# Kernel optimization log

Measured on AMD Instinct MI355X. Metric: run time of the kernel, lower is better.

Reference implementation:

```python
import jax, jax.numpy as jnp
import numpy as np


def setup_inputs() -> dict:
    key = jax.random.key(0)
    k1, k2, k3 = jax.random.split(key, 3)
    N, D, H, E = 8192, 1024, 1024, 16
    scale = 1.0 / np.sqrt(D)
    return {
        "x": jax.random.normal(k1, (N, D), dtype=jnp.float32),
        "router_w": jax.random.normal(k2, (D, E), dtype=jnp.float32) * scale,
        "router_b": jnp.zeros((E,), dtype=jnp.float32),
        "expert_w": jax.random.normal(k3, (E, D, H), dtype=jnp.float32) * scale,
        "expert_b": jnp.zeros((E, H), dtype=jnp.float32),
        "k": 2,
    }


def reference(x, router_w, router_b, expert_w, expert_b, k):
    # Router: softmax over experts, then top-k.
    logits = x @ router_w + router_b                      # [N, E]
    routing_weights = jax.nn.softmax(logits, axis=-1)     # [N, E]
    top_k_weights, top_k_indices = jax.lax.top_k(routing_weights, k)  # [N, k]

    # Dense all-expert compute (faithful to original): [N, E, H]
    expert_outputs = jnp.einsum('nd,edh->neh', x, expert_w) + expert_b[None, :, :]

    # Gather top-k expert outputs: [N, k, H]
    gathered = jnp.take_along_axis(expert_outputs, top_k_indices[:, :, None], axis=1)

    # Weighted sum over k (weights NOT renormalized, as in the original).
    out = jnp.sum(top_k_weights[:, :, None] * gathered, axis=1)  # [N, H]
    return out
```

## Files before the change

kernel.cpp:

```cpp
#include <hip/hip_runtime.h>
#include <hip/hip_bf16.h>


#define N_TOK 8192
#define D_DIM 1024
#define H_DIM 1024
#define E_NUM 16
#define CAP   1024
#define KPAD  40

typedef __attribute__((ext_vector_type(4))) float f32x4;
typedef __attribute__((ext_vector_type(8))) short bf16x8;

__device__ __forceinline__ unsigned short f2bf(float f) {
    unsigned int u = __float_as_uint(f);
    unsigned int r = u + 0x7fffu + ((u >> 16) & 1u);
    return (unsigned short)(r >> 16);
}
__device__ __forceinline__ unsigned int pk2bf(float lo, float hi) {
    return (unsigned int)f2bf(lo) | ((unsigned int)f2bf(hi) << 16);
}

__global__ __launch_bounds__(256, 4) void router_kernel(
    const float* __restrict__ x,
    const float* __restrict__ rw,
    const float* __restrict__ rb,
    int4* __restrict__ res)
{
    const int wave = threadIdx.x >> 6;
    const int lane = threadIdx.x & 63;
    const int ds   = lane >> 4;
    const int e    = lane & 15;
    const int t0   = blockIdx.x * 8 + wave * 2;

    const float* x0  = x + (size_t)t0 * D_DIM + ds * 256;
    const float* x1  = x0 + D_DIM;
    const float* rwp = rw + ds * 4096 + e;

    double acc0 = 0.0, acc1 = 0.0;
#pragma unroll 2
    for (int g = 0; g < 8; ++g) {
        float s0 = 0.0f, s1 = 0.0f;
#pragma unroll
        for (int u = 0; u < 8; ++u) {
            const int jb = g * 8 + u;
            const float4 a = *(const float4*)(x0 + jb * 4);
            const float4 b = *(const float4*)(x1 + jb * 4);
            const float w0 = rwp[jb * 64];
            const float w1 = rwp[jb * 64 + 16];
            const float w2 = rwp[jb * 64 + 32];
            const float w3 = rwp[jb * 64 + 48];
            s0 = fmaf(a.w, w3, fmaf(a.z, w2, fmaf(a.y, w1, fmaf(a.x, w0, s0))));
            s1 = fmaf(b.w, w3, fmaf(b.z, w2, fmaf(b.y, w1, fmaf(b.x, w0, s1))));
        }
        acc0 += (double)s0;
        acc1 += (double)s1;
    }

    double v0 = acc0, v1 = acc1;
    v0 += __shfl_xor(v0, 16); v0 += __shfl_xor(v0, 32);
    v1 += __shfl_xor(v1, 16); v1 += __shfl_xor(v1, 32);

    __shared__ double lg[4][2][E_NUM];
    if (ds == 0) {
        const double bias = (double)rb[e];
        lg[wave][0][e] = v0 + bias;
        lg[wave][1][e] = v1 + bias;
    }
    __syncthreads();

    if (lane < 2) {
        const double* L = lg[wave][lane];
        double m = L[0];
#pragma unroll
        for (int k = 1; k < E_NUM; ++k) m = fmax(m, L[k]);

        int e1 = 0;
#pragma unroll
        for (int k = 1; k < E_NUM; ++k) if (L[k] > L[e1]) e1 = k;
        int e2 = (e1 == 0) ? 1 : 0;
        for (int k = 0; k < E_NUM; ++k)
            if (k != e1 && L[k] > L[e2]) e2 = k;

        float s = 0.0f;
#pragma unroll
        for (int k = 0; k < E_NUM; ++k) s = fmaf(expf((float)(L[k] - m)), 1.0f, s);
        const float w1 = expf((float)(L[e1] - m)) / s;
        const float w2 = expf((float)(L[e2] - m)) / s;

        const int n = t0 + lane;
        res[n] = make_int4(e1, e2, __float_as_int(w1), __float_as_int(w2));
    }
}

__global__ __launch_bounds__(256) void build_lists(
    const int4* __restrict__ res,
    int* __restrict__ counts0, int* __restrict__ counts1,
    int2* __restrict__ entries0, int2* __restrict__ entries1)
{
    const int e = blockIdx.x;
    __shared__ int c0, c1;
    if (threadIdx.x == 0) { c0 = 0; c1 = 0; }
    __syncthreads();

    for (int i = threadIdx.x; i < N_TOK; i += 256) {
        const int4 r = res[i];
        if (r.x == e) {
            int p = atomicAdd(&c0, 1);
            if (p < CAP) entries0[e * CAP + p] = make_int2(i, r.z);
        }
        if (r.y == e) {
            int p = atomicAdd(&c1, 1);
            if (p < CAP) entries1[e * CAP + p] = make_int2(i, r.w);
        }
    }
    __syncthreads();
    if (threadIdx.x == 0) { counts0[e] = c0; counts1[e] = c1; }
}

template <bool ADD>
__global__ __launch_bounds__(256) void moe_mfma_kernel(
    const float* __restrict__ x,
    const float* __restrict__ ew,
    const float* __restrict__ eb,
    const int* __restrict__ counts,
    const int2* __restrict__ entries,
    float* __restrict__ out)
{
    const int flat = blockIdx.x;
    const int lid  = (flat & 7) * 128 + (flat >> 3);
    const int h0 = (lid & 7) * 128;
    const int i0 = ((lid >> 3) & 7) * 128;
    const int e  = lid >> 6;

    int count = counts[e];
    if (count > CAP) count = CAP;
    if (i0 >= count) return;

    __shared__ unsigned short Xs[2][128][KPAD];
    __shared__ unsigned short Ws[2][128][KPAD];
    __shared__ int   s_tok[128];
    __shared__ float s_w[128];

    const int tid = threadIdx.x;
    if (tid < 128) {
        const int i = i0 + tid;
        if (i < count) {
            int2 en = entries[e * CAP + i];
            s_tok[tid] = en.x;
            s_w[tid] = __int_as_float(en.y);
        } else {
            s_tok[tid] = 0;
            s_w[tid] = 0.0f;
        }
    }
    __syncthreads();

    const int wave = tid >> 6;
    const int lane = tid & 63;
    const int wr = (wave >> 1) * 64;
    const int wc = (wave & 1) * 64;
    const int l15 = lane & 15;
    const int quad = lane >> 4;

    f32x4 acc[4][4] = {};

    const int a_kq = (tid & 7) * 4;
    const int a_r0 = tid >> 3;
    const int b_n  = tid & 127;
    const int b_dh = (tid >> 7) * 16;

    const float* ap[4];
#pragma unroll
    for (int it = 0; it < 4; ++it)
        ap[it] = x + (size_t)s_tok[a_r0 + it * 32] * D_DIM + a_kq;
    const float* bp = ew + (size_t)e * D_DIM * H_DIM
                    + (size_t)b_dh * H_DIM + h0 + b_n;

    float4 pa[4];
    float  pb[16];
#pragma unroll
    for (int it = 0; it < 4; ++it) pa[it] = *(const float4*)(ap[it]);
#pragma unroll
    for (int i = 0; i < 16; ++i)  pb[i] = bp[(size_t)i * H_DIM];

    {
#pragma unroll
        for (int it = 0; it < 4; ++it) {
            ushort4 p;
            p.x = f2bf(pa[it].x); p.y = f2bf(pa[it].y);
            p.z = f2bf(pa[it].z); p.w = f2bf(pa[it].w);
            *(ushort4*)&Xs[0][a_r0 + it * 32][a_kq] = p;
        }
        uint4 lo, hi;
        lo.x = pk2bf(pb[0], pb[1]);   lo.y = pk2bf(pb[2], pb[3]);
        lo.z = pk2bf(pb[4], pb[5]);   lo.w = pk2bf(pb[6], pb[7]);
        hi.x = pk2bf(pb[8], pb[9]);   hi.y = pk2bf(pb[10], pb[11]);
        hi.z = pk2bf(pb[12], pb[13]); hi.w = pk2bf(pb[14], pb[15]);
        *(uint4*)&Ws[0][b_n][b_dh]     = lo;
        *(uint4*)&Ws[0][b_n][b_dh + 8] = hi;
    }

    int cur = 0;
    for (int d0 = 0; d0 < D_DIM; d0 += 32) {
        __syncthreads();
        const bool more = (d0 + 32 < D_DIM);

        if (more) {
#pragma unroll
            for (int it = 0; it < 4; ++it)
                pa[it] = *(const float4*)(ap[it] + d0 + 32);
#pragma unroll
            for (int i = 0; i < 16; ++i)
                pb[i] = bp[(size_t)(d0 + 32 + i) * H_DIM];
        }

        bf16x8 af[4], bq[4];
#pragma unroll
        for (int i = 0; i < 4; ++i)
            af[i] = *(const bf16x8*)&Xs[cur][wr + i * 16 + l15][quad * 8];
#pragma unroll
        for (int j = 0; j < 4; ++j)
            bq[j] = *(const bf16x8*)&Ws[cur][wc + j * 16 + l15][quad * 8];
#pragma unroll
        for (int i = 0; i < 4; ++i)
#pragma unroll
            for (int j = 0; j < 4; ++j)
                acc[i][j] = __builtin_amdgcn_mfma_f32_16x16x32_bf16(
                    af[i], bq[j], acc[i][j], 0, 0, 0);

        if (more) {
            const int nxt = cur ^ 1;
#pragma unroll
            for (int it = 0; it < 4; ++it) {
                ushort4 p;
                p.x = f2bf(pa[it].x); p.y = f2bf(pa[it].y);
                p.z = f2bf(pa[it].z); p.w = f2bf(pa[it].w);
                *(ushort4*)&Xs[nxt][a_r0 + it * 32][a_kq] = p;
            }
            uint4 lo, hi;
            lo.x = pk2bf(pb[0], pb[1]);   lo.y = pk2bf(pb[2], pb[3]);
            lo.z = pk2bf(pb[4], pb[5]);   lo.w = pk2bf(pb[6], pb[7]);
            hi.x = pk2bf(pb[8], pb[9]);   hi.y = pk2bf(pb[10], pb[11]);
            hi.z = pk2bf(pb[12], pb[13]); hi.w = pk2bf(pb[14], pb[15]);
            *(uint4*)&Ws[nxt][b_n][b_dh]     = lo;
            *(uint4*)&Ws[nxt][b_n][b_dh + 8] = hi;
        }
        cur ^= 1;
    }

    float bias_j[4];
    const float* ebp = eb + e * H_DIM + h0 + wc;
#pragma unroll
    for (int j = 0; j < 4; ++j) bias_j[j] = ebp[j * 16 + l15];

#pragma unroll
    for (int i = 0; i < 4; ++i) {
#pragma unroll
        for (int r = 0; r < 4; ++r) {
            const int row = wr + i * 16 + quad * 4 + r;
            if (i0 + row < count) {
                const int tok = s_tok[row];
                const float w = s_w[row];
                float* op = out + (size_t)tok * H_DIM + h0 + wc + l15;
#pragma unroll
                for (int j = 0; j < 4; ++j) {
                    float v = w * (acc[i][j][r] + bias_j[j]);
                    if (ADD) v += op[j * 16];
                    op[j * 16] = v;
                }
            }
        }
    }
}

extern "C" void kernel_launch(void* const* d_in, const int* in_sizes, int n_in,
                              void* d_out, int out_size, void* d_ws, size_t ws_size,
                              hipStream_t stream)
{
    const float* x  = (const float*)d_in[0];
    const float* rw = (const float*)d_in[1];
    const float* rb = (const float*)d_in[2];
    const float* ew = (const float*)d_in[3];
    const float* eb = (const float*)d_in[4];

    char* ws = (char*)d_ws;
    int*  counts0  = (int*)ws;
    int*  counts1  = (int*)(ws + 64);
    int2* entries0 = (int2*)(ws + 1024);
    int2* entries1 = (int2*)(ws + 1024 + E_NUM * CAP * 8);

    int4* res = (int4*)d_out;

    router_kernel<<<N_TOK / 8, 256, 0, stream>>>(x, rw, rb, res);

    build_lists<<<E_NUM, 256, 0, stream>>>(res, counts0, counts1,
                                           entries0, entries1);

    moe_mfma_kernel<false><<<1024, 256, 0, stream>>>(
        x, ew, eb, counts0, entries0, (float*)d_out);
    moe_mfma_kernel<true><<<1024, 256, 0, stream>>>(
        x, ew, eb, counts1, entries1, (float*)d_out);
}
```

Baseline: 330.4 us.

## Pre-convert inputs and transposed expert weights to bf16 before grouped GEMM

Adds a conversion kernel that writes x as bf16 and each expert's weight matrix transposed to bf16 in workspace. The expert GEMMs then load pre-converted bf16 tiles directly instead of converting fp32 to bf16 inside the inner loop. Blocks are assigned only to occupied expert tiles through a prefix walk over the counts. This adds an extra full pass over x and all expert weights (about 96MB read, 48MB written) and needs a large workspace; otherwise it falls back to the old path.

```diff
diff --git a/kernel.cpp b/kernel.cpp
--- a/kernel.cpp
+++ b/kernel.cpp
@@ -116,6 +116,181 @@
     }
     __syncthreads();
     if (threadIdx.x == 0) { counts0[e] = c0; counts1[e] = c1; }
+}
+
+__global__ __launch_bounds__(256) void cvt_kernel(
+    const float* __restrict__ x,
+    const float* __restrict__ ew,
+    unsigned short* __restrict__ xb,
+    unsigned short* __restrict__ wt)
+{
+    const int tid = threadIdx.x;
+    if (blockIdx.x < 4096) {
+        const size_t base = ((size_t)blockIdx.x * 256 + tid) * 8;
+        const float4 a = *(const float4*)(x + base);
+        const float4 b = *(const float4*)(x + base + 4);
+        uint4 p;
+        p.x = pk2bf(a.x, a.y); p.y = pk2bf(a.z, a.w);
+        p.z = pk2bf(b.x, b.y); p.w = pk2bf(b.z, b.w);
+        *(uint4*)(xb + base) = p;
+        return;
+    }
+    __shared__ unsigned short Ts[64][68];
+    const int wi = blockIdx.x - 4096;
+    const int e  = wi >> 8;
+    const int kt = (wi >> 4) & 15;
+    const int ht = wi & 15;
+
+    {
+        const int kl0 = tid >> 4;
+        const int hl  = (tid & 15) * 4;
+        const float* src = ew + (size_t)e * (D_DIM * H_DIM)
+                         + (size_t)(kt * 64 + kl0) * H_DIM + ht * 64 + hl;
+#pragma unroll
+        for (int i = 0; i < 4; ++i) {
+            const float4 v = *(const float4*)(src + (size_t)i * 16 * H_DIM);
+            ushort4 p;
+            p.x = f2bf(v.x); p.y = f2bf(v.y); p.z = f2bf(v.z); p.w = f2bf(v.w);
+            *(ushort4*)&Ts[kl0 + i * 16][hl] = p;
+        }
+    }
+    __syncthreads();
+    {
+        const int h2 = tid >> 2;
+        const int kc = (tid & 3) * 16;
+        unsigned int r[8];
+#pragma unroll
+        for (int i = 0; i < 8; ++i)
+            r[i] = (unsigned int)Ts[kc + 2 * i][h2]
+                 | ((unsigned int)Ts[kc + 2 * i + 1][h2] << 16);
+        unsigned short* dst = wt + (size_t)e * (D_DIM * H_DIM)
+                            + (size_t)(ht * 64 + h2) * D_DIM + kt * 64 + kc;
+        *(uint4*)dst       = *(uint4*)&r[0];
+        *(uint4*)(dst + 8) = *(uint4*)&r[4];
+    }
+}
+
+template <bool ADD>
+__global__ __launch_bounds__(256) void moe_gemm_bf16(
+    const unsigned short* __restrict__ xb,
+    const unsigned short* __restrict__ wt,
+    const float* __restrict__ eb,
+    const int* __restrict__ counts,
+    const int2* __restrict__ entries,
+    float* __restrict__ out)
+{
+    int e = 0, loc = blockIdx.x, count = 0;
+    for (; e < E_NUM; ++e) {
+        int c = counts[e]; if (c > CAP) c = CAP;
+        const int nb = ((c + 127) >> 7) << 3;
+        if (loc < nb) { count = c; break; }
+        loc -= nb;
+    }
+    if (e == E_NUM) return;
+    const int i0 = (loc >> 3) * 128;
+    const int h0 = (loc & 7) * 128;
+
+    __shared__ unsigned short Xs[2][128][KPAD];
+    __shared__ unsigned short Ws[2][128][KPAD];
+    __shared__ int   s_tok[128];
+    __shared__ float s_w[128];
+
+    const int tid = threadIdx.x;
+    if (tid < 128) {
+        const int i = i0 + tid;
+        if (i < count) {
+            int2 en = entries[e * CAP + i];
+            s_tok[tid] = en.x;
+            s_w[tid] = __int_as_float(en.y);
+        } else {
+            s_tok[tid] = 0;
+            s_w[tid] = 0.0f;
+        }
+    }
+    __syncthreads();
+
+    const int wave = tid >> 6;
+    const int lane = tid & 63;
+    const int wr = (wave >> 1) * 64;
+    const int wc = (wave & 1) * 64;
+    const int l15 = lane & 15;
+    const int quad = lane >> 4;
+
+    f32x4 acc[4][4] = {};
+
+    const int row  = tid >> 1;
+    const int half = (tid & 1) * 16;
+    const unsigned short* xp = xb + (size_t)s_tok[row] * D_DIM + half;
+    const unsigned short* wp = wt + (size_t)(e * H_DIM + h0 + row) * D_DIM + half;
+
+    uint4 pa0 = *(const uint4*)(xp);
+    uint4 pa1 = *(const uint4*)(xp + 8);
+    uint4 pw0 = *(const uint4*)(wp);
+    uint4 pw1 = *(const uint4*)(wp + 8);
+    *(uint4*)&Xs[0][row][half]     = pa0;
+    *(uint4*)&Xs[0][row][half + 8] = pa1;
+    *(uint4*)&Ws[0][row][half]     = pw0;
+    *(uint4*)&Ws[0][row][half + 8] = pw1;
+
+    int cur = 0;
+    for (int d0 = 0; d0 < D_DIM; d0 += 32) {
+        __syncthreads();
+        const bool more = (d0 + 32 < D_DIM);
+
+        if (more) {
+            pa0 = *(const uint4*)(xp + d0 + 32);
+            pa1 = *(const uint4*)(xp + d0 + 40);
+            pw0 = *(const uint4*)(wp + d0 + 32);
+            pw1 = *(const uint4*)(wp + d0 + 40);
+        }
+
+        bf16x8 af[4], bq[4];
+#pragma unroll
+        for (int i = 0; i < 4; ++i)
+            af[i] = *(const bf16x8*)&Xs[cur][wr + i * 16 + l15][quad * 8];
+#pragma unroll
+        for (int j = 0; j < 4; ++j)
+            bq[j] = *(const bf16x8*)&Ws[cur][wc + j * 16 + l15][quad * 8];
+#pragma unroll
+        for (int i = 0; i < 4; ++i)
+#pragma unroll
+            for (int j = 0; j < 4; ++j)
+                acc[i][j] = __builtin_amdgcn_mfma_f32_16x16x32_bf16(
+                    af[i], bq[j], acc[i][j], 0, 0, 0);
+
+        if (more) {
+            const int nxt = cur ^ 1;
+            *(uint4*)&Xs[nxt][row][half]     = pa0;
+            *(uint4*)&Xs[nxt][row][half + 8] = pa1;
+            *(uint4*)&Ws[nxt][row][half]     = pw0;
+            *(uint4*)&Ws[nxt][row][half + 8] = pw1;
+        }
+        cur ^= 1;
+    }
+
+    float bias_j[4];
+    const float* ebp = eb + e * H_DIM + h0 + wc;
+#pragma unroll
+    for (int j = 0; j < 4; ++j) bias_j[j] = ebp[j * 16 + l15];
+
+#pragma unroll
+    for (int i = 0; i < 4; ++i) {
+#pragma unroll
+        for (int r = 0; r < 4; ++r) {
+            const int orow = wr + i * 16 + quad * 4 + r;
+            if (i0 + orow < count) {
+                const int tok = s_tok[orow];
+                const float w = s_w[orow];
+                float* op = out + (size_t)tok * H_DIM + h0 + wc + l15;
+#pragma unroll
+                for (int j = 0; j < 4; ++j) {
+                    float v = w * (acc[i][j][r] + bias_j[j]);
+                    if (ADD) v += op[j * 16];
+                    op[j * 16] = v;
+                }
+            }
+        }
+    }
 }
 
 template <bool ADD>
@@ -258,10 +433,10 @@
     for (int i = 0; i < 4; ++i) {
 #pragma unroll
         for (int r = 0; r < 4; ++r) {
-            const int row = wr + i * 16 + quad * 4 + r;
-            if (i0 + row < count) {
-                const int tok = s_tok[row];
-                const float w = s_w[row];
+            const int orow = wr + i * 16 + quad * 4 + r;
+            if (i0 + orow < count) {
+                const int tok = s_tok[orow];
+                const float w = s_w[orow];
                 float* op = out + (size_t)tok * H_DIM + h0 + wc + l15;
 #pragma unroll
                 for (int j = 0; j < 4; ++j) {
@@ -290,6 +465,12 @@
     int2* entries0 = (int2*)(ws + 1024);
     int2* entries1 = (int2*)(ws + 1024 + E_NUM * CAP * 8);
 
+    const size_t XB_OFF = (size_t)1 << 20;
+    const size_t XB_SZ  = (size_t)N_TOK * D_DIM * 2;
+    const size_t WT_OFF = XB_OFF + XB_SZ;
+    const size_t WT_SZ  = (size_t)E_NUM * D_DIM * H_DIM * 2;
+    const bool precache = ws_size >= WT_OFF + WT_SZ;
+
     int4* res = (int4*)d_out;
 
     router_kernel<<<N_TOK / 8, 256, 0, stream>>>(x, rw, rb, res);
@@ -297,8 +478,18 @@
     build_lists<<<E_NUM, 256, 0, stream>>>(res, counts0, counts1,
                                            entries0, entries1);
 
-    moe_mfma_kernel<false><<<1024, 256, 0, stream>>>(
-        x, ew, eb, counts0, entries0, (float*)d_out);
-    moe_mfma_kernel<true><<<1024, 256, 0, stream>>>(
-        x, ew, eb, counts1, entries1, (float*)d_out);
-}
+    if (precache) {
+        unsigned short* xbp = (unsigned short*)(ws + XB_OFF);
+        unsigned short* wtp = (unsigned short*)(ws + WT_OFF);
+        cvt_kernel<<<8192, 256, 0, stream>>>(x, ew, xbp, wtp);
+        moe_gemm_bf16<false><<<1024, 256, 0, stream>>>(
+            xbp, wtp, eb, counts0, entries0, (float*)d_out);
+        moe_gemm_bf16<true><<<1024, 256, 0, stream>>>(
+            xbp, wtp, eb, counts1, entries1, (float*)d_out);
+    } else {
+        moe_mfma_kernel<false><<<1024, 256, 0, stream>>>(
+            x, ew, eb, counts0, entries0, (float*)d_out);
+        moe_mfma_kernel<true><<<1024, 256, 0, stream>>>(
+            x, ew, eb, counts1, entries1, (float*)d_out);
+    }
+}
```

Result: faster. 285.3 us (-13.7%).
